# Kernel tuning notes

Measured on AMD Instinct MI355X. Metric: run time of the kernel, lower is better.

## Reference

```python
import jax, jax.numpy as jnp
import numpy as np

T, B, S = 50, 64, 100
H, C = 512, 512
V_TGT, V_EXT = 32000, 5000
UNK = 0  # ext_dict.stoi[UNK_WORD]


def setup_inputs() -> dict:
    key = jax.random.key(0)
    ks = jax.random.split(key, 8)
    return {
        "hidden": jax.random.normal(ks[0], (T, B, H), jnp.float32),
        "dec_rnn_output": jax.random.normal(ks[1], (T, B, H), jnp.float32),
        "concat_c": jax.random.normal(ks[2], (T, B, H + C), jnp.float32),
        "attn": jax.random.uniform(ks[3], (T, B, S), jnp.float32),
        "copy_to_ext": jax.random.randint(ks[4], (S, B), 0, V_EXT, jnp.int64),
        "W": jax.random.normal(ks[5], (V_TGT, H), jnp.float32) * 0.02,
        "b": jnp.zeros((V_TGT,), jnp.float32),
        "Wc": jax.random.normal(ks[6], (1, H), jnp.float32) * 0.02,
        "bc": jnp.zeros((1,), jnp.float32),
    }


def _safe_log(v):
    return jnp.log(jnp.clip(v, 0.001, 1.0 - 0.001))


def reference(hidden, dec_rnn_output, concat_c, attn, copy_to_ext, W, b, Wc, bc):
    # standard softmax over tgt vocab
    logits = jnp.einsum("tbh,vh->tbv", hidden, W) + b          # [T,B,V_TGT]
    prob_log = jax.nn.log_softmax(logits, axis=-1)
    # copy gate p(z) from decoder hidden (copy_prb == 'hidden')
    copy = jax.nn.sigmoid(jnp.einsum("tbh,oh->tbo", dec_rnn_output, Wc) + bc)  # [T,B,1]
    mul_attn = attn * (1.0 - copy)                              # [T,B,S]
    # onehot+bmm == masked scatter-add of attn mass into ext-vocab bins
    mask = (copy_to_ext != UNK).astype(mul_attn.dtype)          # [S,B]
    aw = mul_attn * mask.T[None]                                # [T,B,S]

    def scatter_one(a_ts, idx_s):  # a_ts [T,S], idx_s [S]
        return jnp.zeros((T, V_EXT), a_ts.dtype).at[:, idx_s].add(a_ts)

    ext_copy_prob = jax.vmap(scatter_one, in_axes=(1, 1), out_axes=1)(aw, copy_to_ext)  # [T,B,V_EXT]
    ext_copy_prob_log = _safe_log(ext_copy_prob)
    return jnp.concatenate([prob_log, ext_copy_prob_log], axis=-1)  # [T,B,V_TGT+V_EXT]
```

## Files before the change

kernel.cpp:

```cpp
#include <hip/hip_runtime.h>
#include <hip/hip_bf16.h>

#define TT 50
#define BB 64
#define SS 100
#define HH 512
#define VT 32000
#define VE 5000
#define LDC 37000
#define MROWS 3200
#define NTILE 125
#define NRT 25
#define NWG 3125
#define TSTR 136

typedef __bf16 bf16x8 __attribute__((ext_vector_type(8)));
typedef float f32x4 __attribute__((ext_vector_type(4)));

__device__ __forceinline__ ushort f2bf(float f) {
    unsigned u = __float_as_uint(f);
    u += 0x7fffu + ((u >> 16) & 1u);
    return (ushort)(u >> 16);
}
__device__ __forceinline__ float bflo(unsigned u) { return __uint_as_float(u << 16); }
__device__ __forceinline__ float bfhi(unsigned u) { return __uint_as_float(u & 0xffff0000u); }

__global__ void convert_kernel(const float* __restrict__ W, const float* __restrict__ hid,
                               ushort* __restrict__ wsB, ushort* __restrict__ wsA) {
    int g = blockIdx.x * 256 + threadIdx.x;
    const int WG = 4096000;
    float4 v;
    ushort* dst;
    if (g < WG) {
        v = ((const float4*)W)[g];
        dst = wsB + 4 * (size_t)g;
    } else {
        int h = g - WG;
        v = ((const float4*)hid)[h];
        dst = wsA + 4 * (size_t)h;
    }
    ushort4 o;
    o.x = f2bf(v.x); o.y = f2bf(v.y); o.z = f2bf(v.z); o.w = f2bf(v.w);
    *(ushort4*)dst = o;
}

__global__ __launch_bounds__(256, 2) void gemm_kernel(const ushort* __restrict__ A,
                                                      const ushort* __restrict__ B,
                                                      const float* __restrict__ bias,
                                                      ushort* __restrict__ stash, int sstr,
                                                      float* __restrict__ pm,
                                                      float* __restrict__ ps) {
    __shared__ char smem[49152];
    const int tid  = threadIdx.x;
    const int w    = tid >> 6;
    const int lane = tid & 63;
    const int wr   = w >> 1, wc = w & 1;
    const int lr   = lane & 15;
    const int kg   = lane >> 4;
    const int kgs  = kg ^ ((lr >> 1) & 3);

    const int orig = blockIdx.x;
    const int xcd  = orig & 7, seq = orig >> 3;
    const int wgid = (xcd < 5 ? xcd * 391 : 5 * 391 + (xcd - 5) * 390) + seq;
    const int ct   = wgid / NRT;
    const int rt   = wgid - ct * NRT;
    const int brow = rt * 128;
    const int bcol = ct * 256;

    ushort* tileT = (ushort*)smem;
    const int a0 = tid, a1 = tid + 256;
    const int ar0 = a0 >> 2, as0 = (a0 & 3) ^ ((ar0 >> 1) & 3);
    const int ar1 = a1 >> 2, as1 = (a1 & 3) ^ ((ar1 >> 1) & 3);

    f32x4 acc[4][8];
#pragma unroll
    for (int m = 0; m < 4; ++m)
#pragma unroll
        for (int n = 0; n < 8; ++n)
            acc[m][n] = (f32x4){0.f, 0.f, 0.f, 0.f};

#define STAGE(buf, kt)                                                                      \
    do {                                                                                    \
        char* bA = smem + (buf) * 24576;                                                    \
        char* bB = smem + (buf) * 24576 + 8192;                                             \
        __builtin_amdgcn_global_load_lds(                                                   \
            (const __attribute__((address_space(1))) void*)(A + (size_t)(brow + ar0) * HH + (kt) * 32 + as0 * 8), \
            (__attribute__((address_space(3))) void*)(bA + a0 * 16), 16, 0, 0);             \
        __builtin_amdgcn_global_load_lds(                                                   \
            (const __attribute__((address_space(1))) void*)(A + (size_t)(brow + ar1) * HH + (kt) * 32 + as1 * 8), \
            (__attribute__((address_space(3))) void*)(bA + a1 * 16), 16, 0, 0);             \
        _Pragma("unroll")                                                                   \
        for (int j = 0; j < 4; ++j) {                                                       \
            int c = tid + j * 256;                                                          \
            int row = c >> 2, kcs = (c & 3) ^ ((row >> 1) & 3);                             \
            __builtin_amdgcn_global_load_lds(                                               \
                (const __attribute__((address_space(1))) void*)(B + (size_t)(bcol + row) * HH + (kt) * 32 + kcs * 8), \
                (__attribute__((address_space(3))) void*)(bB + c * 16), 16, 0, 0);          \
        }                                                                                   \
    } while (0)

    STAGE(0, 0);
    for (int kt = 0; kt < 16; ++kt) {
        const int cur = kt & 1;
        if (kt < 15) {
            STAGE(cur ^ 1, kt + 1);
            asm volatile("s_waitcnt vmcnt(6)" ::: "memory");
        } else {
            asm volatile("s_waitcnt vmcnt(0)" ::: "memory");
        }
        __builtin_amdgcn_sched_barrier(0);
        __builtin_amdgcn_s_barrier();
        __builtin_amdgcn_sched_barrier(0);

        const char* pa = smem + cur * 24576;
        const char* pb = smem + cur * 24576 + 8192;
        bf16x8 af[4], bfr[8];
#pragma unroll
        for (int m = 0; m < 4; ++m)
            af[m] = *(const bf16x8*)(pa + (wr * 64 + m * 16 + lr) * 64 + kgs * 16);
#pragma unroll
        for (int n = 0; n < 8; ++n)
            bfr[n] = *(const bf16x8*)(pb + (wc * 128 + n * 16 + lr) * 64 + kgs * 16);
        __builtin_amdgcn_sched_barrier(0);
        __builtin_amdgcn_s_setprio(1);
#pragma unroll
        for (int m = 0; m < 4; ++m)
#pragma unroll
            for (int n = 0; n < 8; ++n)
                acc[m][n] = __builtin_amdgcn_mfma_f32_16x16x32_bf16(af[m], bfr[n], acc[m][n], 0, 0, 0);
        __builtin_amdgcn_s_setprio(0);
        __builtin_amdgcn_sched_barrier(0);
        __builtin_amdgcn_s_barrier();
    }
#undef STAGE
    __syncthreads();

    const int prow = tid >> 1, phalf = tid & 1;
    float Mx = -1e30f, Sx = 0.f;
#pragma unroll
    for (int h = 0; h < 2; ++h) {
        if (wc == h) {
#pragma unroll
            for (int n = 0; n < 8; ++n) {
                int col = n * 16 + lr;
                float bv = bias[bcol + h * 128 + col];
#pragma unroll
                for (int m = 0; m < 4; ++m) {
                    int row0 = wr * 64 + m * 16 + kg * 4;
#pragma unroll
                    for (int r = 0; r < 4; ++r)
                        tileT[(row0 + r) * TSTR + col] = f2bf(acc[m][n][r] + bv);
                }
            }
        }
        __syncthreads();

#pragma unroll
        for (int it = 0; it < 8; ++it) {
            int idx = it * 256 + tid;
            int row = idx >> 4, ch = idx & 15;
            uint4 v = *(const uint4*)(&tileT[row * TSTR + ch * 8]);
            *(uint4*)(stash + (size_t)(brow + row) * sstr + bcol + h * 128 + ch * 8) = v;
        }

        {
            const ushort* trow = &tileT[prow * TSTR + phalf * 64];
            uint4 vv[8];
#pragma unroll
            for (int i = 0; i < 8; ++i) vv[i] = *(const uint4*)(trow + i * 8);
            float mx = -1e30f;
#pragma unroll
            for (int i = 0; i < 8; ++i) {
                mx = fmaxf(mx, fmaxf(fmaxf(bflo(vv[i].x), bfhi(vv[i].x)), fmaxf(bflo(vv[i].y), bfhi(vv[i].y))));
                mx = fmaxf(mx, fmaxf(fmaxf(bflo(vv[i].z), bfhi(vv[i].z)), fmaxf(bflo(vv[i].w), bfhi(vv[i].w))));
            }
            float sx = 0.f;
#pragma unroll
            for (int i = 0; i < 8; ++i) {
                sx += __expf(bflo(vv[i].x) - mx) + __expf(bfhi(vv[i].x) - mx)
                    + __expf(bflo(vv[i].y) - mx) + __expf(bfhi(vv[i].y) - mx)
                    + __expf(bflo(vv[i].z) - mx) + __expf(bfhi(vv[i].z) - mx)
                    + __expf(bflo(vv[i].w) - mx) + __expf(bfhi(vv[i].w) - mx);
            }
            float nm = fmaxf(Mx, mx);
            Sx = Sx * __expf(Mx - nm) + sx * __expf(mx - nm);
            Mx = nm;
        }
        __syncthreads();
    }

    {
        float om = __shfl_xor(Mx, 1), os = __shfl_xor(Sx, 1);
        float M = fmaxf(Mx, om);
        float S = Sx * __expf(Mx - M) + os * __expf(om - M);
        if (phalf == 0) {
            pm[(size_t)ct * MROWS + brow + prow] = M;
            ps[(size_t)ct * MROWS + brow + prow] = S;
        }
    }
}

__global__ __launch_bounds__(256) void norm_ext_kernel(float* __restrict__ out,
                                                       const ushort* __restrict__ stash,
                                                       int sstr, int inplace,
                                                       const float* __restrict__ pm,
                                                       const float* __restrict__ ps,
                                                       const float* __restrict__ dec,
                                                       const float* __restrict__ wc,
                                                       const float* __restrict__ bcp,
                                                       const float* __restrict__ attn,
                                                       const int* __restrict__ cte) {
    const int r = blockIdx.x;
    const int t = threadIdx.x;
    const int w = t >> 6, lane = t & 63;
    __shared__ float sm[4], ssv[4], red[4];
    __shared__ float lse_sh, csh;
    __shared__ float bins[VE];

    float m = -1e30f, s = 0.f;
    if (t < NTILE) {
        m = pm[(size_t)t * MROWS + r];
        s = ps[(size_t)t * MROWS + r];
    }
    for (int off = 1; off < 64; off <<= 1) {
        float om = __shfl_xor(m, off), os = __shfl_xor(s, off);
        float nm = fmaxf(m, om);
        s = s * __expf(m - nm) + os * __expf(om - nm);
        m = nm;
    }
    if (lane == 0) { sm[w] = m; ssv[w] = s; }

    {
        float part = dec[(size_t)r * HH + t] * wc[t]
                   + dec[(size_t)r * HH + t + 256] * wc[t + 256];
        for (int off = 1; off < 64; off <<= 1) part += __shfl_xor(part, off);
        if (lane == 0) red[w] = part;
    }
    for (int v = t; v < VE; v += 256) bins[v] = 0.f;
    __syncthreads();

    if (t == 0) {
        float M = sm[0], S = ssv[0];
        for (int i = 1; i < 4; ++i) {
            float nm = fmaxf(M, sm[i]);
            S = S * __expf(M - nm) + ssv[i] * __expf(sm[i] - nm);
            M = nm;
        }
        lse_sh = M + __logf(S);
        float g = red[0] + red[1] + red[2] + red[3] + bcp[0];
        csh = 1.f / (1.f + __expf(-g));
    }
    __syncthreads();
    const float l = lse_sh;
    const float c = csh;

    if (t < SS) {
        float aw = attn[(size_t)r * SS + t] * (1.f - c);
        int idx = cte[t * BB + (r & 63)];
        if (idx != 0) atomicAdd(&bins[idx], aw);
    }

    const uint4* gsrc = (const uint4*)(stash + (size_t)r * sstr);
    float4* orow = (float4*)(out + (size_t)r * LDC);
    if (inplace) {
        for (int n = 0; n < 16; ++n) {
            int i = t + 256 * n;
            if (i < VT / 8) {
                uint4 v = gsrc[i];
                float4 a, b;
                a.x = bflo(v.x) - l; a.y = bfhi(v.x) - l;
                a.z = bflo(v.y) - l; a.w = bfhi(v.y) - l;
                b.x = bflo(v.z) - l; b.y = bfhi(v.z) - l;
                b.z = bflo(v.w) - l; b.w = bfhi(v.w) - l;
                orow[2 * i]     = a;
                orow[2 * i + 1] = b;
            }
            if ((n & 1) == 1) __syncthreads();
        }
    } else {
        for (int i = t; i < VT / 8; i += 256) {
            uint4 v = gsrc[i];
            float4 a, b;
            a.x = bflo(v.x) - l; a.y = bfhi(v.x) - l;
            a.z = bflo(v.y) - l; a.w = bfhi(v.y) - l;
            b.x = bflo(v.z) - l; b.y = bfhi(v.z) - l;
            b.z = bflo(v.w) - l; b.w = bfhi(v.w) - l;
            orow[2 * i]     = a;
            orow[2 * i + 1] = b;
        }
    }
    __syncthreads();

    float4* eo = (float4*)(out + (size_t)r * LDC + VT);
    for (int v = t; v < VE / 4; v += 256) {
        float4 x;
        x.x = __logf(fminf(fmaxf(bins[4 * v + 0], 0.001f), 0.999f));
        x.y = __logf(fminf(fmaxf(bins[4 * v + 1], 0.001f), 0.999f));
        x.z = __logf(fminf(fmaxf(bins[4 * v + 2], 0.001f), 0.999f));
        x.w = __logf(fminf(fmaxf(bins[4 * v + 3], 0.001f), 0.999f));
        eo[v] = x;
    }
}

extern "C" void kernel_launch(void* const* d_in, const int* in_sizes, int n_in,
                              void* d_out, int out_size, void* d_ws, size_t ws_size,
                              hipStream_t stream) {
    const float* hidden = (const float*)d_in[0];
    const float* dec    = (const float*)d_in[1];
    const float* attn   = (const float*)d_in[3];
    const int*   cte    = (const int*)d_in[4];
    const float* W      = (const float*)d_in[5];
    const float* bias   = (const float*)d_in[6];
    const float* Wc     = (const float*)d_in[7];
    const float* bc     = (const float*)d_in[8];
    float* out = (float*)d_out;

    ushort* wsB = (ushort*)d_ws;
    ushort* wsA = wsB + (size_t)VT * HH;
    float*  pm  = (float*)(wsA + (size_t)MROWS * HH);
    float*  ps  = pm + (size_t)NTILE * MROWS;

    const size_t base_off = (size_t)VT * HH * 2 + (size_t)MROWS * HH * 2
                          + 2ull * NTILE * MROWS * 4;
    const size_t base_al  = (base_off + 127) & ~(size_t)127;
    const size_t stash_bytes = (size_t)MROWS * VT * 2;
    ushort* stash;
    int sstr, inplace;
    if (ws_size >= base_al + stash_bytes) {
        stash = (ushort*)((char*)d_ws + base_al);
        sstr = VT;
        inplace = 0;
    } else {
        stash = (ushort*)out + 42000;
        sstr = 74000;
        inplace = 1;
    }

    convert_kernel<<<17600, 256, 0, stream>>>(W, hidden, wsB, wsA);
    gemm_kernel<<<NWG, 256, 0, stream>>>(wsA, wsB, bias, stash, sstr, pm, ps);
    norm_ext_kernel<<<MROWS, 256, 0, stream>>>(out, stash, sstr, inplace,
                                               pm, ps, dec, Wc, bc, attn, cte);
}
```

Measured before the change: 337.9 us.

## Triple-buffer GEMM K-loop and compute softmax stats from fp32 registers

The GEMM main loop moves from double to triple buffering in LDS. Loads now run two K-steps ahead, and the trailing barrier in each iteration is dropped, leaving one barrier per step. The per-tile row max and sum-exp are now computed directly from the fp32 accumulators with lane shuffles and a small LDS merge, instead of re-reading the bf16 tile from LDS after staging. This raises LDS use to 72KB per block, which may limit occupancy. The stats now come from unrounded fp32 logits rather than the bf16 values that are stored.

```diff
diff --git a/kernel.cpp b/kernel.cpp
--- a/kernel.cpp
+++ b/kernel.cpp
@@ -50,7 +50,7 @@
                                                       ushort* __restrict__ stash, int sstr,
                                                       float* __restrict__ pm,
                                                       float* __restrict__ ps) {
-    __shared__ char smem[49152];
+    __shared__ char smem[73728];
     const int tid  = threadIdx.x;
     const int w    = tid >> 6;
     const int lane = tid & 63;
@@ -79,10 +79,12 @@
         for (int n = 0; n < 8; ++n)
             acc[m][n] = (f32x4){0.f, 0.f, 0.f, 0.f};
 
-#define STAGE(buf, kt)                                                                      \
+#define SLOTA(s) (smem + (s) * 24576)
+#define SLOTB(s) (smem + (s) * 24576 + 8192)
+#define STAGE(s, kt)                                                                        \
     do {                                                                                    \
-        char* bA = smem + (buf) * 24576;                                                    \
-        char* bB = smem + (buf) * 24576 + 8192;                                             \
+        char* bA = SLOTA(s);                                                                \
+        char* bB = SLOTB(s);                                                                \
         __builtin_amdgcn_global_load_lds(                                                   \
             (const __attribute__((address_space(1))) void*)(A + (size_t)(brow + ar0) * HH + (kt) * 32 + as0 * 8), \
             (__attribute__((address_space(3))) void*)(bA + a0 * 16), 16, 0, 0);             \
@@ -99,11 +101,10 @@
         }                                                                                   \
     } while (0)
 
-    STAGE(0, 0);
+    STAGE(0, 0); STAGE(1, 1);
+    int slot = 0;
     for (int kt = 0; kt < 16; ++kt) {
-        const int cur = kt & 1;
         if (kt < 15) {
-            STAGE(cur ^ 1, kt + 1);
             asm volatile("s_waitcnt vmcnt(6)" ::: "memory");
         } else {
             asm volatile("s_waitcnt vmcnt(0)" ::: "memory");
@@ -112,8 +113,13 @@
         __builtin_amdgcn_s_barrier();
         __builtin_amdgcn_sched_barrier(0);
 
-        const char* pa = smem + cur * 24576;
-        const char* pb = smem + cur * 24576 + 8192;
+        if (kt < 14) {
+            const int sl2 = (slot + 2 >= 3) ? slot - 1 : slot + 2;
+            STAGE(sl2, kt + 2);
+        }
+
+        const char* pa = (const char*)SLOTA(slot);
+        const char* pb = (const char*)SLOTB(slot);
         bf16x8 af[4], bfr[8];
 #pragma unroll
         for (int m = 0; m < 4; ++m)
@@ -130,31 +136,80 @@
                 acc[m][n] = __builtin_amdgcn_mfma_f32_16x16x32_bf16(af[m], bfr[n], acc[m][n], 0, 0, 0);
         __builtin_amdgcn_s_setprio(0);
         __builtin_amdgcn_sched_barrier(0);
-        __builtin_amdgcn_s_barrier();
+
+        slot = (slot == 2) ? 0 : slot + 1;
     }
 #undef STAGE
-    __syncthreads();
-
-    const int prow = tid >> 1, phalf = tid & 1;
-    float Mx = -1e30f, Sx = 0.f;
+#undef SLOTA
+#undef SLOTB
+    __syncthreads();
+
+    float bv[8];
+#pragma unroll
+    for (int n = 0; n < 8; ++n) bv[n] = bias[bcol + wc * 128 + n * 16 + lr];
+
+    float* pmx = (float*)(smem + 69632);
+    float* psx = pmx + 256;
+#pragma unroll
+    for (int m = 0; m < 4; ++m) {
+        float mxr[4] = {-1e30f, -1e30f, -1e30f, -1e30f};
+#pragma unroll
+        for (int n = 0; n < 8; ++n)
+#pragma unroll
+            for (int r = 0; r < 4; ++r)
+                mxr[r] = fmaxf(mxr[r], acc[m][n][r] + bv[n]);
+#pragma unroll
+        for (int off = 1; off < 16; off <<= 1)
+#pragma unroll
+            for (int r = 0; r < 4; ++r)
+                mxr[r] = fmaxf(mxr[r], __shfl_xor(mxr[r], off));
+        float sxr[4] = {0.f, 0.f, 0.f, 0.f};
+#pragma unroll
+        for (int n = 0; n < 8; ++n)
+#pragma unroll
+            for (int r = 0; r < 4; ++r)
+                sxr[r] += __expf(acc[m][n][r] + bv[n] - mxr[r]);
+#pragma unroll
+        for (int off = 1; off < 16; off <<= 1)
+#pragma unroll
+            for (int r = 0; r < 4; ++r)
+                sxr[r] += __shfl_xor(sxr[r], off);
+        if (lr == 0) {
+#pragma unroll
+            for (int r = 0; r < 4; ++r) {
+                int row = wr * 64 + m * 16 + kg * 4 + r;
+                pmx[row * 2 + wc] = mxr[r];
+                psx[row * 2 + wc] = sxr[r];
+            }
+        }
+    }
+    __syncthreads();
+
+    if (tid < 128) {
+        float m0 = pmx[tid * 2], m1 = pmx[tid * 2 + 1];
+        float s0 = psx[tid * 2], s1 = psx[tid * 2 + 1];
+        float M = fmaxf(m0, m1);
+        float S = s0 * __expf(m0 - M) + s1 * __expf(m1 - M);
+        pm[(size_t)ct * MROWS + brow + tid] = M;
+        ps[(size_t)ct * MROWS + brow + tid] = S;
+    }
+
 #pragma unroll
     for (int h = 0; h < 2; ++h) {
         if (wc == h) {
 #pragma unroll
             for (int n = 0; n < 8; ++n) {
                 int col = n * 16 + lr;
-                float bv = bias[bcol + h * 128 + col];
 #pragma unroll
                 for (int m = 0; m < 4; ++m) {
                     int row0 = wr * 64 + m * 16 + kg * 4;
 #pragma unroll
                     for (int r = 0; r < 4; ++r)
-                        tileT[(row0 + r) * TSTR + col] = f2bf(acc[m][n][r] + bv);
+                        tileT[(row0 + r) * TSTR + col] = f2bf(acc[m][n][r] + bv[n]);
                 }
             }
         }
         __syncthreads();
-
 #pragma unroll
         for (int it = 0; it < 8; ++it) {
             int idx = it * 256 + tid;
@@ -162,41 +217,7 @@
             uint4 v = *(const uint4*)(&tileT[row * TSTR + ch * 8]);
             *(uint4*)(stash + (size_t)(brow + row) * sstr + bcol + h * 128 + ch * 8) = v;
         }
-
-        {
-            const ushort* trow = &tileT[prow * TSTR + phalf * 64];
-            uint4 vv[8];
-#pragma unroll
-            for (int i = 0; i < 8; ++i) vv[i] = *(const uint4*)(trow + i * 8);
-            float mx = -1e30f;
-#pragma unroll
-            for (int i = 0; i < 8; ++i) {
-                mx = fmaxf(mx, fmaxf(fmaxf(bflo(vv[i].x), bfhi(vv[i].x)), fmaxf(bflo(vv[i].y), bfhi(vv[i].y))));
-                mx = fmaxf(mx, fmaxf(fmaxf(bflo(vv[i].z), bfhi(vv[i].z)), fmaxf(bflo(vv[i].w), bfhi(vv[i].w))));
-            }
-            float sx = 0.f;
-#pragma unroll
-            for (int i = 0; i < 8; ++i) {
-                sx += __expf(bflo(vv[i].x) - mx) + __expf(bfhi(vv[i].x) - mx)
-                    + __expf(bflo(vv[i].y) - mx) + __expf(bfhi(vv[i].y) - mx)
-                    + __expf(bflo(vv[i].z) - mx) + __expf(bfhi(vv[i].z) - mx)
-                    + __expf(bflo(vv[i].w) - mx) + __expf(bfhi(vv[i].w) - mx);
-            }
-            float nm = fmaxf(Mx, mx);
-            Sx = Sx * __expf(Mx - nm) + sx * __expf(mx - nm);
-            Mx = nm;
-        }
         __syncthreads();
-    }
-
-    {
-        float om = __shfl_xor(Mx, 1), os = __shfl_xor(Sx, 1);
-        float M = fmaxf(Mx, om);
-        float S = Sx * __expf(Mx - M) + os * __expf(om - M);
-        if (phalf == 0) {
-            pm[(size_t)ct * MROWS + brow + prow] = M;
-            ps[(size_t)ct * MROWS + brow + prow] = S;
-        }
     }
 }
 
```

After: 346.8 us. +2.6%, slower.

## Load A fragments directly into registers instead of staging through LDS

Applied to the files above, without the earlier changes.

The A operand tiles are no longer copied into shared memory. Each wave now loads its own A fragments straight from global memory into registers, double-buffered across K iterations, while B still goes through LDS via async global-to-LDS loads. This shrinks LDS use from 48KB to 34KB and removes the A LDS reads, which could allow more resident workgroups. In exchange it adds register pressure, and A rows are fetched redundantly by the two waves sharing a row band with less coalesced access.

```diff
diff --git a/kernel.cpp b/kernel.cpp
--- a/kernel.cpp
+++ b/kernel.cpp
@@ -50,7 +50,7 @@
                                                       ushort* __restrict__ stash, int sstr,
                                                       float* __restrict__ pm,
                                                       float* __restrict__ ps) {
-    __shared__ char smem[49152];
+    __shared__ char smem[34816];
     const int tid  = threadIdx.x;
     const int w    = tid >> 6;
     const int lane = tid & 63;
@@ -68,9 +68,6 @@
     const int bcol = ct * 256;
 
     ushort* tileT = (ushort*)smem;
-    const int a0 = tid, a1 = tid + 256;
-    const int ar0 = a0 >> 2, as0 = (a0 & 3) ^ ((ar0 >> 1) & 3);
-    const int ar1 = a1 >> 2, as1 = (a1 & 3) ^ ((ar1 >> 1) & 3);
 
     f32x4 acc[4][8];
 #pragma unroll
@@ -79,16 +76,11 @@
         for (int n = 0; n < 8; ++n)
             acc[m][n] = (f32x4){0.f, 0.f, 0.f, 0.f};
 
-#define STAGE(buf, kt)                                                                      \
+    bf16x8 rA0[4], rA1[4];
+
+#define STAGE_B(buf, kt)                                                                    \
     do {                                                                                    \
-        char* bA = smem + (buf) * 24576;                                                    \
-        char* bB = smem + (buf) * 24576 + 8192;                                             \
-        __builtin_amdgcn_global_load_lds(                                                   \
-            (const __attribute__((address_space(1))) void*)(A + (size_t)(brow + ar0) * HH + (kt) * 32 + as0 * 8), \
-            (__attribute__((address_space(3))) void*)(bA + a0 * 16), 16, 0, 0);             \
-        __builtin_amdgcn_global_load_lds(                                                   \
-            (const __attribute__((address_space(1))) void*)(A + (size_t)(brow + ar1) * HH + (kt) * 32 + as1 * 8), \
-            (__attribute__((address_space(3))) void*)(bA + a1 * 16), 16, 0, 0);             \
+        char* bB = smem + (buf) * 16384;                                                    \
         _Pragma("unroll")                                                                   \
         for (int j = 0; j < 4; ++j) {                                                       \
             int c = tid + j * 256;                                                          \
@@ -99,40 +91,55 @@
         }                                                                                   \
     } while (0)
 
-    STAGE(0, 0);
-    for (int kt = 0; kt < 16; ++kt) {
-        const int cur = kt & 1;
-        if (kt < 15) {
-            STAGE(cur ^ 1, kt + 1);
-            asm volatile("s_waitcnt vmcnt(6)" ::: "memory");
-        } else {
-            asm volatile("s_waitcnt vmcnt(0)" ::: "memory");
-        }
-        __builtin_amdgcn_sched_barrier(0);
-        __builtin_amdgcn_s_barrier();
-        __builtin_amdgcn_sched_barrier(0);
-
-        const char* pa = smem + cur * 24576;
-        const char* pb = smem + cur * 24576 + 8192;
-        bf16x8 af[4], bfr[8];
-#pragma unroll
-        for (int m = 0; m < 4; ++m)
-            af[m] = *(const bf16x8*)(pa + (wr * 64 + m * 16 + lr) * 64 + kgs * 16);
-#pragma unroll
-        for (int n = 0; n < 8; ++n)
-            bfr[n] = *(const bf16x8*)(pb + (wc * 128 + n * 16 + lr) * 64 + kgs * 16);
-        __builtin_amdgcn_sched_barrier(0);
-        __builtin_amdgcn_s_setprio(1);
-#pragma unroll
-        for (int m = 0; m < 4; ++m)
-#pragma unroll
-            for (int n = 0; n < 8; ++n)
-                acc[m][n] = __builtin_amdgcn_mfma_f32_16x16x32_bf16(af[m], bfr[n], acc[m][n], 0, 0, 0);
-        __builtin_amdgcn_s_setprio(0);
-        __builtin_amdgcn_sched_barrier(0);
-        __builtin_amdgcn_s_barrier();
-    }
-#undef STAGE
+#define LOADA(dst, kt)                                                                      \
+    do {                                                                                    \
+        _Pragma("unroll")                                                                   \
+        for (int m = 0; m < 4; ++m)                                                         \
+            dst[m] = *(const bf16x8*)(A + (size_t)(brow + wr * 64 + m * 16 + lr) * HH       \
+                                        + (kt) * 32 + kg * 8);                              \
+    } while (0)
+
+#define ITER(kt, CUR, NXT)                                                                  \
+    do {                                                                                    \
+        if ((kt) < 15) {                                                                    \
+            STAGE_B(((kt) + 1) & 1, (kt) + 1);    \
+            LOADA(NXT, (kt) + 1);                 \
+            asm volatile("s_waitcnt vmcnt(8)" ::: "memory");          \
+        } else {                                                                            \
+            asm volatile("s_waitcnt vmcnt(0)" ::: "memory");                                \
+        }                                                                                   \
+        __builtin_amdgcn_sched_barrier(0);                                                  \
+        __builtin_amdgcn_s_barrier();                    \
+        __builtin_amdgcn_sched_barrier(0);                                                  \
+        {                                                                                   \
+            const char* pb = smem + ((kt) & 1) * 16384;                                     \
+            bf16x8 bfr[8];                                                                  \
+            _Pragma("unroll")                                                               \
+            for (int n = 0; n < 8; ++n)                                                     \
+                bfr[n] = *(const bf16x8*)(pb + (wc * 128 + n * 16 + lr) * 64 + kgs * 16);   \
+            __builtin_amdgcn_sched_barrier(0);                                              \
+            __builtin_amdgcn_s_setprio(1);                                                  \
+            _Pragma("unroll")                                                               \
+            for (int m = 0; m < 4; ++m)                                                     \
+                _Pragma("unroll")                                                           \
+                for (int n = 0; n < 8; ++n)                                                 \
+                    acc[m][n] = __builtin_amdgcn_mfma_f32_16x16x32_bf16(CUR[m], bfr[n],     \
+                                                                        acc[m][n], 0, 0, 0);\
+            __builtin_amdgcn_s_setprio(0);                                                  \
+            __builtin_amdgcn_sched_barrier(0);                                              \
+        }                                                                                   \
+        __builtin_amdgcn_s_barrier();                   \
+    } while (0)
+
+    STAGE_B(0, 0);
+    LOADA(rA0, 0);
+    for (int kt2 = 0; kt2 < 16; kt2 += 2) {
+        ITER(kt2, rA0, rA1);
+        ITER(kt2 + 1, rA1, rA0);
+    }
+#undef ITER
+#undef LOADA
+#undef STAGE_B
     __syncthreads();
 
     const int prow = tid >> 1, phalf = tid & 1;
```

Measured after the change: 374.4 us. +10.8%, slower.
